# Performance work log

Hardware: AMD Instinct MI355X
Metric: run time of the kernel (lower is better)

Reference implementation:

```python
import jax, jax.numpy as jnp
import numpy as np

N_NODES = 50000
N_EDGES = 600000
D = 128
LAYERS = 2


def setup_inputs() -> dict:
    key = jax.random.key(0)
    ks = jax.random.split(key, 7)
    row = jax.random.randint(ks[0], (N_EDGES,), 0, N_NODES, dtype=jnp.int32)
    col = jax.random.randint(ks[1], (N_EDGES,), 0, N_NODES, dtype=jnp.int32)
    vals = jax.random.normal(ks[2], (N_EDGES,), dtype=jnp.float32)
    X = jax.random.normal(ks[3], (N_NODES, D), dtype=jnp.float32)
    temps = jax.random.normal(ks[4], (LAYERS, D), dtype=jnp.float32) * 0.1
    W = jax.random.normal(ks[5], (LAYERS, D, D), dtype=jnp.float32) * (1.0 / np.sqrt(D))
    b = jax.random.normal(ks[6], (LAYERS, D), dtype=jnp.float32) * 0.01
    return {"row": row, "col": col, "vals": vals, "X": X, "temps": temps, "W": W, "b": b}


def reference(row, col, vals, X, temps, W, b):
    # Iterated: X <- relu(Linear_i(X - temp_i * (Lap @ X)))
    for i in range(LAYERS):
        # spmm via COO edge list: LX[r] = sum_e vals[e] * X[col[e]] for edges with row[e]==r
        msgs = vals[:, None] * X[col]            # [E, D] gather + scale
        LX = jax.ops.segment_sum(msgs, row, num_segments=N_NODES)  # [N, D] scatter-add
        X = X - temps[i] * LX                    # elementwise scale-subtract
        X = jax.nn.relu(X @ W[i].T + b[i])       # Linear (torch: x W^T + b) + ReLU
    return X
```

## Files before the change

kernel.cpp:

```cpp
#include <hip/hip_runtime.h>

#define N_NODES 50000
#define N_EDGES 600000
#define D 128
#define LAYERS 2
#define NAL 50048
#define CAP 48

typedef short bf16x8 __attribute__((ext_vector_type(8)));
typedef float f32x4 __attribute__((ext_vector_type(4)));
typedef float f32x2 __attribute__((ext_vector_type(2)));

__device__ __forceinline__ ushort f2b(float f) {
  uint u = __float_as_uint(f);
  return (ushort)((u + 0x7fffu + ((u >> 16) & 1u)) >> 16);
}
__device__ __forceinline__ float b2f_lo(uint p) { return __uint_as_float(p << 16); }
__device__ __forceinline__ float b2f_hi(uint p) { return __uint_as_float(p & 0xffff0000u); }

__global__ void k_prep(const float* __restrict__ X, const float* __restrict__ W,
                       int* __restrict__ counts, ushort* __restrict__ Xb,
                       ushort* __restrict__ Wb, uint* __restrict__ Xf8) {
  int i = blockIdx.x * 256 + threadIdx.x;
  if (i < NAL) counts[i] = 0;
  if (i < N_NODES * D / 4) {
    float4 v = ((const float4*)X)[i];
    ushort4 o;
    o.x = f2b(v.x); o.y = f2b(v.y); o.z = f2b(v.z); o.w = f2b(v.w);
    ((ushort4*)Xb)[i] = o;
    int pk = __builtin_amdgcn_cvt_pk_fp8_f32(v.x, v.y, 0, false);
    pk = __builtin_amdgcn_cvt_pk_fp8_f32(v.z, v.w, pk, true);
    Xf8[i] = (uint)pk;
  }
  if (i < LAYERS * D * D / 4) {
    float4 v = ((const float4*)W)[i];
    ushort4 o;
    o.x = f2b(v.x); o.y = f2b(v.y); o.z = f2b(v.z); o.w = f2b(v.w);
    ((ushort4*)Wb)[i] = o;
  }
}

__global__ void k_fill_ell(const int* __restrict__ row, const int* __restrict__ col,
                           const float* __restrict__ vals, int* __restrict__ counts,
                           uint* __restrict__ ell) {
  int e = blockIdx.x * 256 + threadIdx.x;
  if (e < N_EDGES) {
    int r = row[e];
    int pos = atomicAdd(&counts[r], 1);
    if (pos < CAP)
      ell[(size_t)r * CAP + pos] = ((uint)f2b(vals[e]) << 16) | (uint)col[e];
  }
}

__global__ __launch_bounds__(256) void k_layer(
    const int* __restrict__ counts, const uint* __restrict__ ell,
    const ushort* __restrict__ Xin, const uchar* __restrict__ Xg8,
    const ushort* __restrict__ Wb, const float* __restrict__ bias,
    const float* __restrict__ temps_l,
    ushort* __restrict__ Yb, uchar* __restrict__ Yf8,
    float* __restrict__ Yf, int store_f32) {
  __shared__ ushort Xs[16][136];
  const int t = threadIdx.x;

  {
    const int nloc = t >> 4;
    const int c = t & 15;
    const int g = blockIdx.x * 16 + nloc;
    const uint* ep = ell + (size_t)g * CAP;
    int cnt = counts[g];
    if (cnt > CAP) cnt = CAP;
    float a0 = 0.f, a1 = 0.f, a2 = 0.f, a3 = 0.f;
    float a4 = 0.f, a5 = 0.f, a6 = 0.f, a7 = 0.f;
#define EDGE_FMA(v, q)                                                  \
    {                                                                   \
      f32x2 f0 = __builtin_amdgcn_cvt_pk_f32_fp8((q).x, false);         \
      f32x2 f1 = __builtin_amdgcn_cvt_pk_f32_fp8((q).x, true);          \
      f32x2 f2 = __builtin_amdgcn_cvt_pk_f32_fp8((q).y, false);         \
      f32x2 f3 = __builtin_amdgcn_cvt_pk_f32_fp8((q).y, true);          \
      a0 = fmaf(v, f0.x, a0); a1 = fmaf(v, f0.y, a1);                   \
      a2 = fmaf(v, f1.x, a2); a3 = fmaf(v, f1.y, a3);                   \
      a4 = fmaf(v, f2.x, a4); a5 = fmaf(v, f2.y, a5);                   \
      a6 = fmaf(v, f3.x, a6); a7 = fmaf(v, f3.y, a7);                   \
    }
    uint4 eb = *(const uint4*)ep;
    int j = 0;
    for (; j + 4 <= cnt; j += 4) {
      uint4 en = *(const uint4*)(ep + j + 4);
      uint2 q0 = *(const uint2*)(Xg8 + ((size_t)(eb.x & 0xFFFFu) << 7) + c * 8);
      uint2 q1 = *(const uint2*)(Xg8 + ((size_t)(eb.y & 0xFFFFu) << 7) + c * 8);
      uint2 q2 = *(const uint2*)(Xg8 + ((size_t)(eb.z & 0xFFFFu) << 7) + c * 8);
      uint2 q3 = *(const uint2*)(Xg8 + ((size_t)(eb.w & 0xFFFFu) << 7) + c * 8);
      float v0 = b2f_hi(eb.x), v1 = b2f_hi(eb.y);
      float v2 = b2f_hi(eb.z), v3 = b2f_hi(eb.w);
      EDGE_FMA(v0, q0); EDGE_FMA(v1, q1); EDGE_FMA(v2, q2); EDGE_FMA(v3, q3);
      eb = en;
    }
    for (; j < cnt; ++j) {
      uint e = ep[j];
      uint2 q = *(const uint2*)(Xg8 + ((size_t)(e & 0xFFFFu) << 7) + c * 8);
      float v = b2f_hi(e);
      EDGE_FMA(v, q);
    }
#undef EDGE_FMA
    uint4 pr = *(const uint4*)(Xin + ((size_t)g << 7) + c * 8);
    float4 t0 = *(const float4*)(temps_l + c * 8);
    float4 t1 = *(const float4*)(temps_l + c * 8 + 4);
    uint r0 = (uint)f2b(b2f_lo(pr.x) - t0.x * a0) | ((uint)f2b(b2f_hi(pr.x) - t0.y * a1) << 16);
    uint r1 = (uint)f2b(b2f_lo(pr.y) - t0.z * a2) | ((uint)f2b(b2f_hi(pr.y) - t0.w * a3) << 16);
    uint r2 = (uint)f2b(b2f_lo(pr.z) - t1.x * a4) | ((uint)f2b(b2f_hi(pr.z) - t1.y * a5) << 16);
    uint r3 = (uint)f2b(b2f_lo(pr.w) - t1.z * a6) | ((uint)f2b(b2f_hi(pr.w) - t1.w * a7) << 16);
    *(uint4*)&Xs[nloc][c * 8] = make_uint4(r0, r1, r2, r3);
  }
  __syncthreads();

  const int wave = t >> 6;
  const int lane = t & 63;
  const int lr = lane & 15;
  const int kg = lane >> 4;

  bf16x8 a0 = *(const bf16x8*)&Xs[lr][0 + kg * 8];
  bf16x8 a1 = *(const bf16x8*)&Xs[lr][32 + kg * 8];
  bf16x8 a2 = *(const bf16x8*)&Xs[lr][64 + kg * 8];
  bf16x8 a3 = *(const bf16x8*)&Xs[lr][96 + kg * 8];

  const int crow = kg * 4;
  #pragma unroll
  for (int q = 0; q < 2; ++q) {
    const int nt = wave * 2 + q;
    const ushort* wp = Wb + ((size_t)(nt * 16 + lr) << 7) + kg * 8;
    bf16x8 b0 = *(const bf16x8*)(wp);
    bf16x8 b1 = *(const bf16x8*)(wp + 32);
    bf16x8 b2 = *(const bf16x8*)(wp + 64);
    bf16x8 b3 = *(const bf16x8*)(wp + 96);
    f32x4 acc = {0.f, 0.f, 0.f, 0.f};
    acc = __builtin_amdgcn_mfma_f32_16x16x32_bf16(a0, b0, acc, 0, 0, 0);
    acc = __builtin_amdgcn_mfma_f32_16x16x32_bf16(a1, b1, acc, 0, 0, 0);
    acc = __builtin_amdgcn_mfma_f32_16x16x32_bf16(a2, b2, acc, 0, 0, 0);
    acc = __builtin_amdgcn_mfma_f32_16x16x32_bf16(a3, b3, acc, 0, 0, 0);
    const int col = nt * 16 + lr;
    const float bv = bias[col];
    if (store_f32) {
      #pragma unroll
      for (int r = 0; r < 4; ++r) {
        int grow = blockIdx.x * 16 + crow + r;
        if (grow < N_NODES)
          Yf[((size_t)grow << 7) + col] = fmaxf(acc[r] + bv, 0.f);
      }
    } else {
      #pragma unroll
      for (int r = 0; r < 4; ++r) {
        int grow = blockIdx.x * 16 + crow + r;
        float o = fmaxf(acc[r] + bv, 0.f);
        Yb[((size_t)grow << 7) + col] = f2b(o);
        int pk = __builtin_amdgcn_cvt_pk_fp8_f32(o, o, 0, false);
        Yf8[((size_t)grow << 7) + col] = (uchar)(pk & 0xff);
      }
    }
  }
}

extern "C" void kernel_launch(void* const* d_in, const int* in_sizes, int n_in,
                              void* d_out, int out_size, void* d_ws, size_t ws_size,
                              hipStream_t stream) {
  const int*   row   = (const int*)d_in[0];
  const int*   col   = (const int*)d_in[1];
  const float* vals  = (const float*)d_in[2];
  const float* X     = (const float*)d_in[3];
  const float* temps = (const float*)d_in[4];
  const float* W     = (const float*)d_in[5];
  const float* b     = (const float*)d_in[6];
  float* Y = (float*)d_out;

  int*    counts = (int*)d_ws;
  uint*   ell    = (uint*)(counts + NAL);
  ushort* Xb     = (ushort*)(ell + (size_t)NAL * CAP);
  ushort* Yb     = Xb + (size_t)NAL * D;
  ushort* Wb     = Yb + (size_t)NAL * D;
  uchar*  Xf8    = (uchar*)(Wb + LAYERS * D * D);
  uchar*  Yf8    = Xf8 + (size_t)NAL * D;

  const int eblocks = (N_EDGES + 255) / 256;
  const int pblocks = (N_NODES * D / 4 + 255) / 256;
  const int lblocks = NAL / 16;

  k_prep<<<pblocks, 256, 0, stream>>>(X, W, counts, Xb, Wb, (uint*)Xf8);
  k_fill_ell<<<eblocks, 256, 0, stream>>>(row, col, vals, counts, ell);

  k_layer<<<lblocks, 256, 0, stream>>>(counts, ell, Xb, Xf8, Wb, b, temps,
                                       Yb, Yf8, nullptr, 0);
  k_layer<<<lblocks, 256, 0, stream>>>(counts, ell, Yb, Yf8, Wb + D * D, b + D,
                                       temps + D, nullptr, nullptr, Y, 1);
}
```

Measured before the change: 108.7 us.

## Merge ELL fill and X/W conversion into one kernel with split block roles

```diff
diff --git a/kernel.cpp b/kernel.cpp
--- a/kernel.cpp
+++ b/kernel.cpp
@@ -6,6 +6,8 @@
 #define LAYERS 2
 #define NAL 50048
 #define CAP 48
+#define FBLOCKS 586
+#define PBLOCKS 6250
 
 typedef short bf16x8 __attribute__((ext_vector_type(8)));
 typedef float f32x4 __attribute__((ext_vector_type(4)));
@@ -18,37 +20,51 @@
 __device__ __forceinline__ float b2f_lo(uint p) { return __uint_as_float(p << 16); }
 __device__ __forceinline__ float b2f_hi(uint p) { return __uint_as_float(p & 0xffff0000u); }
 
-__global__ void k_prep(const float* __restrict__ X, const float* __restrict__ W,
-                       int* __restrict__ counts, ushort* __restrict__ Xb,
-                       ushort* __restrict__ Wb, uint* __restrict__ Xf8) {
+__global__ void k_zero(int* __restrict__ counts) {
   int i = blockIdx.x * 256 + threadIdx.x;
   if (i < NAL) counts[i] = 0;
-  if (i < N_NODES * D / 4) {
-    float4 v = ((const float4*)X)[i];
-    ushort4 o;
-    o.x = f2b(v.x); o.y = f2b(v.y); o.z = f2b(v.z); o.w = f2b(v.w);
-    ((ushort4*)Xb)[i] = o;
-    int pk = __builtin_amdgcn_cvt_pk_fp8_f32(v.x, v.y, 0, false);
-    pk = __builtin_amdgcn_cvt_pk_fp8_f32(v.z, v.w, pk, true);
-    Xf8[i] = (uint)pk;
-  }
-  if (i < LAYERS * D * D / 4) {
-    float4 v = ((const float4*)W)[i];
-    ushort4 o;
-    o.x = f2b(v.x); o.y = f2b(v.y); o.z = f2b(v.z); o.w = f2b(v.w);
-    ((ushort4*)Wb)[i] = o;
-  }
-}
-
-__global__ void k_fill_ell(const int* __restrict__ row, const int* __restrict__ col,
-                           const float* __restrict__ vals, int* __restrict__ counts,
-                           uint* __restrict__ ell) {
-  int e = blockIdx.x * 256 + threadIdx.x;
-  if (e < N_EDGES) {
-    int r = row[e];
-    int pos = atomicAdd(&counts[r], 1);
-    if (pos < CAP)
-      ell[(size_t)r * CAP + pos] = ((uint)f2b(vals[e]) << 16) | (uint)col[e];
+}
+
+__global__ __launch_bounds__(256) void k_prep_fill(
+    const int* __restrict__ row, const int* __restrict__ col,
+    const float* __restrict__ vals, int* __restrict__ counts,
+    uint* __restrict__ ell,
+    const float* __restrict__ X, const float* __restrict__ W,
+    ushort* __restrict__ Xb, ushort* __restrict__ Wb, uint* __restrict__ Xf8) {
+  const int blk = blockIdx.x;
+  const int t = threadIdx.x;
+  if (blk < FBLOCKS) {
+    int fid = blk * 256 + t;
+    if (fid < N_EDGES / 4) {
+      int4   r4 = ((const int4*)row)[fid];
+      int4   c4 = ((const int4*)col)[fid];
+      float4 v4 = ((const float4*)vals)[fid];
+      int p0 = atomicAdd(&counts[r4.x], 1);
+      int p1 = atomicAdd(&counts[r4.y], 1);
+      int p2 = atomicAdd(&counts[r4.z], 1);
+      int p3 = atomicAdd(&counts[r4.w], 1);
+      if (p0 < CAP) ell[(size_t)r4.x * CAP + p0] = ((uint)f2b(v4.x) << 16) | (uint)c4.x;
+      if (p1 < CAP) ell[(size_t)r4.y * CAP + p1] = ((uint)f2b(v4.y) << 16) | (uint)c4.y;
+      if (p2 < CAP) ell[(size_t)r4.z * CAP + p2] = ((uint)f2b(v4.z) << 16) | (uint)c4.z;
+      if (p3 < CAP) ell[(size_t)r4.w * CAP + p3] = ((uint)f2b(v4.w) << 16) | (uint)c4.w;
+    }
+  } else {
+    int i = (blk - FBLOCKS) * 256 + t;
+    if (i < N_NODES * D / 4) {
+      float4 v = ((const float4*)X)[i];
+      ushort4 o;
+      o.x = f2b(v.x); o.y = f2b(v.y); o.z = f2b(v.z); o.w = f2b(v.w);
+      ((ushort4*)Xb)[i] = o;
+      int pk = __builtin_amdgcn_cvt_pk_fp8_f32(v.x, v.y, 0, false);
+      pk = __builtin_amdgcn_cvt_pk_fp8_f32(v.z, v.w, pk, true);
+      Xf8[i] = (uint)pk;
+    }
+    if (i < LAYERS * D * D / 4) {
+      float4 v = ((const float4*)W)[i];
+      ushort4 o;
+      o.x = f2b(v.x); o.y = f2b(v.y); o.z = f2b(v.z); o.w = f2b(v.w);
+      ((ushort4*)Wb)[i] = o;
+    }
   }
 }
 
@@ -179,12 +195,12 @@
   uchar*  Xf8    = (uchar*)(Wb + LAYERS * D * D);
   uchar*  Yf8    = Xf8 + (size_t)NAL * D;
 
-  const int eblocks = (N_EDGES + 255) / 256;
-  const int pblocks = (N_NODES * D / 4 + 255) / 256;
+  const int zblocks = (NAL + 255) / 256;
   const int lblocks = NAL / 16;
 
-  k_prep<<<pblocks, 256, 0, stream>>>(X, W, counts, Xb, Wb, (uint*)Xf8);
-  k_fill_ell<<<eblocks, 256, 0, stream>>>(row, col, vals, counts, ell);
+  k_zero<<<zblocks, 256, 0, stream>>>(counts);
+  k_prep_fill<<<FBLOCKS + PBLOCKS, 256, 0, stream>>>(row, col, vals, counts, ell,
+                                                     X, W, Xb, Wb, (uint*)Xf8);
 
   k_layer<<<lblocks, 256, 0, stream>>>(counts, ell, Xb, Xf8, Wb, b, temps,
                                        Yb, Yf8, nullptr, 0);
```

New measurement: 114.5 us. 5.3% more time.

## Use 8 threads per node with 16-byte fp8 gathers and 32-node blocks

Applied to the files above, without the earlier changes.

```diff
diff --git a/kernel.cpp b/kernel.cpp
--- a/kernel.cpp
+++ b/kernel.cpp
@@ -59,37 +59,40 @@
     const float* __restrict__ temps_l,
     ushort* __restrict__ Yb, uchar* __restrict__ Yf8,
     float* __restrict__ Yf, int store_f32) {
-  __shared__ ushort Xs[16][136];
+  __shared__ ushort Xs[32][136];
   const int t = threadIdx.x;
 
   {
-    const int nloc = t >> 4;
-    const int c = t & 15;
-    const int g = blockIdx.x * 16 + nloc;
+    const int nloc = t >> 3;
+    const int c = t & 7;
+    const int g = blockIdx.x * 32 + nloc;
     const uint* ep = ell + (size_t)g * CAP;
     int cnt = counts[g];
     if (cnt > CAP) cnt = CAP;
-    float a0 = 0.f, a1 = 0.f, a2 = 0.f, a3 = 0.f;
-    float a4 = 0.f, a5 = 0.f, a6 = 0.f, a7 = 0.f;
+    float a[16];
+    #pragma unroll
+    for (int i = 0; i < 16; ++i) a[i] = 0.f;
 #define EDGE_FMA(v, q)                                                  \
     {                                                                   \
-      f32x2 f0 = __builtin_amdgcn_cvt_pk_f32_fp8((q).x, false);         \
-      f32x2 f1 = __builtin_amdgcn_cvt_pk_f32_fp8((q).x, true);          \
-      f32x2 f2 = __builtin_amdgcn_cvt_pk_f32_fp8((q).y, false);         \
-      f32x2 f3 = __builtin_amdgcn_cvt_pk_f32_fp8((q).y, true);          \
-      a0 = fmaf(v, f0.x, a0); a1 = fmaf(v, f0.y, a1);                   \
-      a2 = fmaf(v, f1.x, a2); a3 = fmaf(v, f1.y, a3);                   \
-      a4 = fmaf(v, f2.x, a4); a5 = fmaf(v, f2.y, a5);                   \
-      a6 = fmaf(v, f3.x, a6); a7 = fmaf(v, f3.y, a7);                   \
+      uint w_[4] = {(q).x, (q).y, (q).z, (q).w};                        \
+      _Pragma("unroll")                                                 \
+      for (int u_ = 0; u_ < 4; ++u_) {                                  \
+        f32x2 flo = __builtin_amdgcn_cvt_pk_f32_fp8(w_[u_], false);     \
+        f32x2 fhi = __builtin_amdgcn_cvt_pk_f32_fp8(w_[u_], true);      \
+        a[u_ * 4 + 0] = fmaf(v, flo.x, a[u_ * 4 + 0]);                  \
+        a[u_ * 4 + 1] = fmaf(v, flo.y, a[u_ * 4 + 1]);                  \
+        a[u_ * 4 + 2] = fmaf(v, fhi.x, a[u_ * 4 + 2]);                  \
+        a[u_ * 4 + 3] = fmaf(v, fhi.y, a[u_ * 4 + 3]);                  \
+      }                                                                 \
     }
     uint4 eb = *(const uint4*)ep;
     int j = 0;
     for (; j + 4 <= cnt; j += 4) {
       uint4 en = *(const uint4*)(ep + j + 4);
-      uint2 q0 = *(const uint2*)(Xg8 + ((size_t)(eb.x & 0xFFFFu) << 7) + c * 8);
-      uint2 q1 = *(const uint2*)(Xg8 + ((size_t)(eb.y & 0xFFFFu) << 7) + c * 8);
-      uint2 q2 = *(const uint2*)(Xg8 + ((size_t)(eb.z & 0xFFFFu) << 7) + c * 8);
-      uint2 q3 = *(const uint2*)(Xg8 + ((size_t)(eb.w & 0xFFFFu) << 7) + c * 8);
+      uint4 q0 = *(const uint4*)(Xg8 + ((size_t)(eb.x & 0xFFFFu) << 7) + c * 16);
+      uint4 q1 = *(const uint4*)(Xg8 + ((size_t)(eb.y & 0xFFFFu) << 7) + c * 16);
+      uint4 q2 = *(const uint4*)(Xg8 + ((size_t)(eb.z & 0xFFFFu) << 7) + c * 16);
+      uint4 q3 = *(const uint4*)(Xg8 + ((size_t)(eb.w & 0xFFFFu) << 7) + c * 16);
       float v0 = b2f_hi(eb.x), v1 = b2f_hi(eb.y);
       float v2 = b2f_hi(eb.z), v3 = b2f_hi(eb.w);
       EDGE_FMA(v0, q0); EDGE_FMA(v1, q1); EDGE_FMA(v2, q2); EDGE_FMA(v3, q3);
@@ -97,19 +100,27 @@
     }
     for (; j < cnt; ++j) {
       uint e = ep[j];
-      uint2 q = *(const uint2*)(Xg8 + ((size_t)(e & 0xFFFFu) << 7) + c * 8);
+      uint4 q = *(const uint4*)(Xg8 + ((size_t)(e & 0xFFFFu) << 7) + c * 16);
       float v = b2f_hi(e);
       EDGE_FMA(v, q);
     }
 #undef EDGE_FMA
-    uint4 pr = *(const uint4*)(Xin + ((size_t)g << 7) + c * 8);
-    float4 t0 = *(const float4*)(temps_l + c * 8);
-    float4 t1 = *(const float4*)(temps_l + c * 8 + 4);
-    uint r0 = (uint)f2b(b2f_lo(pr.x) - t0.x * a0) | ((uint)f2b(b2f_hi(pr.x) - t0.y * a1) << 16);
-    uint r1 = (uint)f2b(b2f_lo(pr.y) - t0.z * a2) | ((uint)f2b(b2f_hi(pr.y) - t0.w * a3) << 16);
-    uint r2 = (uint)f2b(b2f_lo(pr.z) - t1.x * a4) | ((uint)f2b(b2f_hi(pr.z) - t1.y * a5) << 16);
-    uint r3 = (uint)f2b(b2f_lo(pr.w) - t1.z * a6) | ((uint)f2b(b2f_hi(pr.w) - t1.w * a7) << 16);
-    *(uint4*)&Xs[nloc][c * 8] = make_uint4(r0, r1, r2, r3);
+    uint4 pr0 = *(const uint4*)(Xin + ((size_t)g << 7) + c * 16);
+    uint4 pr1 = *(const uint4*)(Xin + ((size_t)g << 7) + c * 16 + 8);
+    float4 t0 = *(const float4*)(temps_l + c * 16);
+    float4 t1 = *(const float4*)(temps_l + c * 16 + 4);
+    float4 t2 = *(const float4*)(temps_l + c * 16 + 8);
+    float4 t3 = *(const float4*)(temps_l + c * 16 + 12);
+    uint w0 = (uint)f2b(b2f_lo(pr0.x) - t0.x * a[0])  | ((uint)f2b(b2f_hi(pr0.x) - t0.y * a[1])  << 16);
+    uint w1 = (uint)f2b(b2f_lo(pr0.y) - t0.z * a[2])  | ((uint)f2b(b2f_hi(pr0.y) - t0.w * a[3])  << 16);
+    uint w2 = (uint)f2b(b2f_lo(pr0.z) - t1.x * a[4])  | ((uint)f2b(b2f_hi(pr0.z) - t1.y * a[5])  << 16);
+    uint w3 = (uint)f2b(b2f_lo(pr0.w) - t1.z * a[6])  | ((uint)f2b(b2f_hi(pr0.w) - t1.w * a[7])  << 16);
+    uint w4 = (uint)f2b(b2f_lo(pr1.x) - t2.x * a[8])  | ((uint)f2b(b2f_hi(pr1.x) - t2.y * a[9])  << 16);
+    uint w5 = (uint)f2b(b2f_lo(pr1.y) - t2.z * a[10]) | ((uint)f2b(b2f_hi(pr1.y) - t2.w * a[11]) << 16);
+    uint w6 = (uint)f2b(b2f_lo(pr1.z) - t3.x * a[12]) | ((uint)f2b(b2f_hi(pr1.z) - t3.y * a[13]) << 16);
+    uint w7 = (uint)f2b(b2f_lo(pr1.w) - t3.z * a[14]) | ((uint)f2b(b2f_hi(pr1.w) - t3.w * a[15]) << 16);
+    *(uint4*)&Xs[nloc][c * 16]     = make_uint4(w0, w1, w2, w3);
+    *(uint4*)&Xs[nloc][c * 16 + 8] = make_uint4(w4, w5, w6, w7);
   }
   __syncthreads();
 
@@ -117,16 +128,17 @@
   const int lane = t & 63;
   const int lr = lane & 15;
   const int kg = lane >> 4;
-
-  bf16x8 a0 = *(const bf16x8*)&Xs[lr][0 + kg * 8];
-  bf16x8 a1 = *(const bf16x8*)&Xs[lr][32 + kg * 8];
-  bf16x8 a2 = *(const bf16x8*)&Xs[lr][64 + kg * 8];
-  bf16x8 a3 = *(const bf16x8*)&Xs[lr][96 + kg * 8];
+  const int rt = (wave >> 1) * 16;
+
+  bf16x8 a0 = *(const bf16x8*)&Xs[rt + lr][0 + kg * 8];
+  bf16x8 a1 = *(const bf16x8*)&Xs[rt + lr][32 + kg * 8];
+  bf16x8 a2 = *(const bf16x8*)&Xs[rt + lr][64 + kg * 8];
+  bf16x8 a3 = *(const bf16x8*)&Xs[rt + lr][96 + kg * 8];
 
   const int crow = kg * 4;
   #pragma unroll
-  for (int q = 0; q < 2; ++q) {
-    const int nt = wave * 2 + q;
+  for (int q = 0; q < 4; ++q) {
+    const int nt = (wave & 1) * 4 + q;
     const ushort* wp = Wb + ((size_t)(nt * 16 + lr) << 7) + kg * 8;
     bf16x8 b0 = *(const bf16x8*)(wp);
     bf16x8 b1 = *(const bf16x8*)(wp + 32);
@@ -142,14 +154,14 @@
     if (store_f32) {
       #pragma unroll
       for (int r = 0; r < 4; ++r) {
-        int grow = blockIdx.x * 16 + crow + r;
+        int grow = blockIdx.x * 32 + rt + crow + r;
         if (grow < N_NODES)
           Yf[((size_t)grow << 7) + col] = fmaxf(acc[r] + bv, 0.f);
       }
     } else {
       #pragma unroll
       for (int r = 0; r < 4; ++r) {
-        int grow = blockIdx.x * 16 + crow + r;
+        int grow = blockIdx.x * 32 + rt + crow + r;
         float o = fmaxf(acc[r] + bv, 0.f);
         Yb[((size_t)grow << 7) + col] = f2b(o);
         int pk = __builtin_amdgcn_cvt_pk_fp8_f32(o, o, 0, false);
@@ -181,7 +193,7 @@
 
   const int eblocks = (N_EDGES + 255) / 256;
   const int pblocks = (N_NODES * D / 4 + 255) / 256;
-  const int lblocks = NAL / 16;
+  const int lblocks = NAL / 32;
 
   k_prep<<<pblocks, 256, 0, stream>>>(X, W, counts, Xb, Wb, (uint*)Xf8);
   k_fill_ell<<<eblocks, 256, 0, stream>>>(row, col, vals, counts, ell);
```

After: 113.5 us. 1.04x slower.

## Build ELL via two-pass shared-memory binning instead of global atomics

Applied to the files above, without the earlier changes.

```diff
diff --git a/kernel.cpp b/kernel.cpp
--- a/kernel.cpp
+++ b/kernel.cpp
@@ -6,6 +6,12 @@
 #define LAYERS 2
 #define NAL 50048
 #define CAP 48
+#define NB1 256
+#define EPB 2344
+#define NBINS 256
+#define BIN_ROWS 196
+#define FRAG_CAP 32
+#define PBLOCKS 6250
 
 typedef short bf16x8 __attribute__((ext_vector_type(8)));
 typedef float f32x4 __attribute__((ext_vector_type(4)));
@@ -18,37 +24,75 @@
 __device__ __forceinline__ float b2f_lo(uint p) { return __uint_as_float(p << 16); }
 __device__ __forceinline__ float b2f_hi(uint p) { return __uint_as_float(p & 0xffff0000u); }
 
-__global__ void k_prep(const float* __restrict__ X, const float* __restrict__ W,
-                       int* __restrict__ counts, ushort* __restrict__ Xb,
-                       ushort* __restrict__ Wb, uint* __restrict__ Xf8) {
-  int i = blockIdx.x * 256 + threadIdx.x;
-  if (i < NAL) counts[i] = 0;
-  if (i < N_NODES * D / 4) {
-    float4 v = ((const float4*)X)[i];
-    ushort4 o;
-    o.x = f2b(v.x); o.y = f2b(v.y); o.z = f2b(v.z); o.w = f2b(v.w);
-    ((ushort4*)Xb)[i] = o;
-    int pk = __builtin_amdgcn_cvt_pk_fp8_f32(v.x, v.y, 0, false);
-    pk = __builtin_amdgcn_cvt_pk_fp8_f32(v.z, v.w, pk, true);
-    Xf8[i] = (uint)pk;
-  }
-  if (i < LAYERS * D * D / 4) {
-    float4 v = ((const float4*)W)[i];
-    ushort4 o;
-    o.x = f2b(v.x); o.y = f2b(v.y); o.z = f2b(v.z); o.w = f2b(v.w);
-    ((ushort4*)Wb)[i] = o;
-  }
-}
-
-__global__ void k_fill_ell(const int* __restrict__ row, const int* __restrict__ col,
-                           const float* __restrict__ vals, int* __restrict__ counts,
-                           uint* __restrict__ ell) {
-  int e = blockIdx.x * 256 + threadIdx.x;
-  if (e < N_EDGES) {
-    int r = row[e];
-    int pos = atomicAdd(&counts[r], 1);
-    if (pos < CAP)
-      ell[(size_t)r * CAP + pos] = ((uint)f2b(vals[e]) << 16) | (uint)col[e];
+__global__ __launch_bounds__(256) void k_bin_prep(
+    const int* __restrict__ row, const int* __restrict__ col,
+    const float* __restrict__ vals,
+    uint2* __restrict__ staging, int* __restrict__ bcnt,
+    const float* __restrict__ X, const float* __restrict__ W,
+    ushort* __restrict__ Xb, ushort* __restrict__ Wb, uint* __restrict__ Xf8) {
+  const int blk = blockIdx.x;
+  const int t = threadIdx.x;
+  if (blk < NB1) {
+    __shared__ int lcur[NBINS];
+    lcur[t] = 0;
+    __syncthreads();
+    const int e0 = blk * EPB;
+    for (int i = t; i < EPB; i += 256) {
+      int e = e0 + i;
+      if (e < N_EDGES) {
+        int r = row[e];
+        int bin = r / BIN_ROWS;
+        int slot = atomicAdd(&lcur[bin], 1);
+        if (slot < FRAG_CAP) {
+          uint cv = ((uint)f2b(vals[e]) << 16) | (uint)col[e];
+          staging[((size_t)blk * NBINS + bin) * FRAG_CAP + slot] =
+              make_uint2(cv, (uint)r);
+        }
+      }
+    }
+    __syncthreads();
+    bcnt[blk * NBINS + t] = min(lcur[t], FRAG_CAP);
+  } else {
+    int i = (blk - NB1) * 256 + t;
+    if (i < N_NODES * D / 4) {
+      float4 v = ((const float4*)X)[i];
+      ushort4 o;
+      o.x = f2b(v.x); o.y = f2b(v.y); o.z = f2b(v.z); o.w = f2b(v.w);
+      ((ushort4*)Xb)[i] = o;
+      int pk = __builtin_amdgcn_cvt_pk_fp8_f32(v.x, v.y, 0, false);
+      pk = __builtin_amdgcn_cvt_pk_fp8_f32(v.z, v.w, pk, true);
+      Xf8[i] = (uint)pk;
+    }
+    if (i < LAYERS * D * D / 4) {
+      float4 v = ((const float4*)W)[i];
+      ushort4 o;
+      o.x = f2b(v.x); o.y = f2b(v.y); o.z = f2b(v.z); o.w = f2b(v.w);
+      ((ushort4*)Wb)[i] = o;
+    }
+  }
+}
+
+__global__ __launch_bounds__(256) void k_scatter(
+    const uint2* __restrict__ staging, const int* __restrict__ bcnt,
+    int* __restrict__ counts, uint* __restrict__ ell) {
+  const int b = blockIdx.x;
+  const int t = threadIdx.x;
+  __shared__ int lcur[BIN_ROWS];
+  for (int i = t; i < BIN_ROWS; i += 256) lcur[i] = 0;
+  __syncthreads();
+  const int rbase = b * BIN_ROWS;
+  const int n = bcnt[t * NBINS + b];
+  const uint2* frag = staging + ((size_t)t * NBINS + b) * FRAG_CAP;
+  for (int k = 0; k < n; ++k) {
+    uint2 E = frag[k];
+    int rl = (int)E.y - rbase;
+    int slot = atomicAdd(&lcur[rl], 1);
+    if (slot < CAP) ell[(size_t)E.y * CAP + slot] = E.x;
+  }
+  __syncthreads();
+  for (int i = t; i < BIN_ROWS; i += 256) {
+    int r = rbase + i;
+    if (r < NAL) counts[r] = lcur[i];
   }
 }
 
@@ -171,20 +215,21 @@
   const float* b     = (const float*)d_in[6];
   float* Y = (float*)d_out;
 
-  int*    counts = (int*)d_ws;
-  uint*   ell    = (uint*)(counts + NAL);
-  ushort* Xb     = (ushort*)(ell + (size_t)NAL * CAP);
-  ushort* Yb     = Xb + (size_t)NAL * D;
-  ushort* Wb     = Yb + (size_t)NAL * D;
-  uchar*  Xf8    = (uchar*)(Wb + LAYERS * D * D);
-  uchar*  Yf8    = Xf8 + (size_t)NAL * D;
-
-  const int eblocks = (N_EDGES + 255) / 256;
-  const int pblocks = (N_NODES * D / 4 + 255) / 256;
+  int*    counts  = (int*)d_ws;
+  int*    bcnt    = counts + NAL;
+  uint2*  staging = (uint2*)(bcnt + NB1 * NBINS);
+  uint*   ell     = (uint*)(staging + (size_t)NB1 * NBINS * FRAG_CAP);
+  ushort* Xb      = (ushort*)(ell + (size_t)NAL * CAP);
+  ushort* Yb      = Xb + (size_t)NAL * D;
+  ushort* Wb      = Yb + (size_t)NAL * D;
+  uchar*  Xf8     = (uchar*)(Wb + LAYERS * D * D);
+  uchar*  Yf8     = Xf8 + (size_t)NAL * D;
+
   const int lblocks = NAL / 16;
 
-  k_prep<<<pblocks, 256, 0, stream>>>(X, W, counts, Xb, Wb, (uint*)Xf8);
-  k_fill_ell<<<eblocks, 256, 0, stream>>>(row, col, vals, counts, ell);
+  k_bin_prep<<<NB1 + PBLOCKS, 256, 0, stream>>>(row, col, vals, staging, bcnt,
+                                                X, W, Xb, Wb, (uint*)Xf8);
+  k_scatter<<<NBINS, 256, 0, stream>>>(staging, bcnt, counts, ell);
 
   k_layer<<<lblocks, 256, 0, stream>>>(counts, ell, Xb, Xf8, Wb, b, temps,
                                        Yb, Yf8, nullptr, 0);
```

After: 91.26 us. 1.19x faster.
